# Performance work log

Measured on AMD Instinct MI355X. Metric: run time of the kernel, lower is better.

The kernel has to match this reference:

```python
import jax, jax.numpy as jnp
import numpy as np

B, S, D, H = 4, 4096, 2048, 256
GAMMA = 1.05


def setup_inputs() -> dict:
    key = jax.random.key(0)
    k1, k2, k3, k4 = jax.random.split(key, 4)
    X = jax.random.normal(k1, (B, S, D), dtype=jnp.float32)
    # nn.Linear(d_model, head_size) weights, stored as (in, out) for x @ W
    scale = 1.0 / np.sqrt(D)
    Wq = jax.random.normal(k2, (D, H), dtype=jnp.float32) * scale
    Wk = jax.random.normal(k3, (D, H), dtype=jnp.float32) * scale
    Wv = jax.random.normal(k4, (D, H), dtype=jnp.float32) * scale
    # decay = log(gamma * ones(head_size))
    decay = jnp.full((H,), np.log(GAMMA), dtype=jnp.float32)
    return {"X": X, "Wq": Wq, "Wk": Wk, "Wv": Wv, "decay": decay}


def reference(X, Wq, Wk, Wv, decay):
    # parallel (training) form of RetNet retention
    b, s, _ = X.shape
    h = Wq.shape[1]
    Q = jnp.einsum('bsd,dh->bsh', X, Wq)
    K = jnp.einsum('bsd,dh->bsh', X, Wk)
    V = jnp.einsum('bsd,dh->bsh', X, Wv)
    idx = jnp.arange(s)
    dist = jnp.abs(idx[:, None] - idx[None, :]).astype(X.dtype)  # [S,S]
    # scalar decay (all head_size entries identical at init; see notes)
    decay_matrix = jnp.exp(-decay[0] * dist)
    causal = jnp.tril(jnp.ones((s, s), dtype=X.dtype))
    decay_matrix = decay_matrix * causal
    scores = jnp.einsum('bsh,bth->bst', Q, K) * decay_matrix  # [B,S,S]
    scores = scores / jnp.asarray(h ** 0.5, dtype=X.dtype)
    out = jnp.einsum('bst,bth->bsh', scores, V)  # [B,S,H]
    return out
```

## Files before the change

kernel.cpp:

```cpp
#include <hip/hip_runtime.h>


typedef unsigned short u16;
typedef __attribute__((ext_vector_type(8))) short bf16x8;
typedef __attribute__((ext_vector_type(4))) float f32x4;

#define S_LEN 4096
#define DMODEL 2048
#define HSZ 256
#define NQKV 768
#define WINDOW 128
#define NT 32

__device__ __forceinline__ u16 f2bf(float f) {
  union { float f; unsigned u; } v; v.f = f;
  unsigned r = v.u + 0x7FFFu + ((v.u >> 16) & 1u);
  return (u16)(r >> 16);
}

__device__ __forceinline__ unsigned cvt2(float lo, float hi) {
  unsigned r;
  asm("v_cvt_pk_bf16_f32 %0, %1, %2" : "=v"(r) : "v"(lo), "v"(hi));
  return r;
}

__device__ __forceinline__ void glds16(const void* g, void* l) {
  __builtin_amdgcn_global_load_lds(
      (const __attribute__((address_space(1))) unsigned int*)g,
      (__attribute__((address_space(3))) unsigned int*)l, 16, 0, 0);
}

#define BAR() __builtin_amdgcn_s_barrier()
#define LGKM0() do { asm volatile("s_waitcnt lgkmcnt(0)" ::: "memory"); \
                     __builtin_amdgcn_sched_barrier(0); } while (0)
#define VM6() do { asm volatile("s_waitcnt vmcnt(6)" ::: "memory"); \
                   __builtin_amdgcn_sched_barrier(0); } while (0)
#define VM2() do { asm volatile("s_waitcnt vmcnt(2)" ::: "memory"); \
                   __builtin_amdgcn_sched_barrier(0); } while (0)
#define VM0() do { asm volatile("s_waitcnt vmcnt(0)" ::: "memory"); \
                   __builtin_amdgcn_sched_barrier(0); } while (0)

__global__ __launch_bounds__(256) void k_transposeW(const float* __restrict__ Wq,
                                                    const float* __restrict__ Wk,
                                                    const float* __restrict__ Wv,
                                                    u16* __restrict__ Wt) {
  __shared__ float s[32][33];
  int bid = blockIdx.x;
  int nt = bid % 24, kt = bid / 24;
  int n0 = nt * 32, k0 = kt * 32;
  const float* W = (n0 < 256) ? Wq : (n0 < 512 ? Wk : Wv);
  int nc = n0 & 255;
  int tx = threadIdx.x & 31, ty = threadIdx.x >> 5;
#pragma unroll
  for (int j = 0; j < 4; j++)
    s[ty + j * 8][tx] = W[(k0 + ty + j * 8) * HSZ + nc + tx];
  __syncthreads();
#pragma unroll
  for (int j = 0; j < 4; j++) {
    int nl = ty + j * 8;
    Wt[(n0 + nl) * DMODEL + k0 + tx] = f2bf(s[tx][nl]);
  }
}

__device__ __forceinline__ bf16x8 ldf(const char* hbase, int r, int ks) {
  return *(const bf16x8*)(hbase + r * 128 + ((ks ^ (r & 7)) << 4));
}
__device__ __forceinline__ void stageB(const u16* Bsrc, char* bufbase, int t,
                                       int cb, int w, int l) {
  int r0 = l >> 3, sl = (l & 7) ^ r0;
  glds16(Bsrc + (size_t)(cb * 64 + w * 8 + r0) * DMODEL + t * 64 + sl * 8,
         bufbase + cb * 8192 + w * 1024);
}
__device__ __forceinline__ void stageA(const float* __restrict__ X, size_t m0,
                                       char* slot, int t, int p, int j,
                                       int w, int l) {
#pragma unroll
  for (int i = 0; i < 2; i++) {
    int call = j * 16 + w * 2 + i;
    int sr = call * 4 + (l >> 4);
    int gs = (l & 15) ^ (sr & 15);
    int grow = ((sr >> 6) << 7) + p * 64 + (sr & 63);
    glds16(X + (m0 + (size_t)grow) * DMODEL + t * 64 + gs * 4,
           slot + call * 1024);
  }
}
__device__ __forceinline__ void readA(const char* slot, int wm, int c, int g,
                                      bf16x8 (&af)[4][2]) {
#pragma unroll
  for (int m = 0; m < 4; m++) {
    int sr = wm * 64 + m * 16 + c;
    const char* rowp = slot + sr * 256;
    int sw = sr & 15;
#pragma unroll
    for (int kc = 0; kc < 2; kc++) {
      int gb = kc * 8 + g * 2;
      float4 fa = *(const float4*)(rowp + ((gb) ^ sw) * 16);
      float4 fb = *(const float4*)(rowp + ((gb + 1) ^ sw) * 16);
      union { bf16x8 v; unsigned u[4]; } o;
      o.u[0] = cvt2(fa.x, fa.y);
      o.u[1] = cvt2(fa.z, fa.w);
      o.u[2] = cvt2(fb.x, fb.y);
      o.u[3] = cvt2(fb.z, fb.w);
      af[m][kc] = o.v;
    }
  }
}
__device__ __forceinline__ void read_b01(const char* Bc, int wn, int c, int g,
                                         bf16x8 (&dst)[2][2]) {
#pragma unroll
  for (int n = 0; n < 2; n++) {
    int r = wn * 48 + n * 16 + c;
    dst[n][0] = ldf(Bc, r, g);
    dst[n][1] = ldf(Bc, r, 4 + g);
  }
}
__device__ __forceinline__ void read_b2(const char* Bc, int wn, int c, int g,
                                        bf16x8 (&dst)[2]) {
  int r = wn * 48 + 32 + c;
  dst[0] = ldf(Bc, r, g);
  dst[1] = ldf(Bc, r, 4 + g);
}
__device__ __forceinline__ void mfma16(const bf16x8 (&A)[4][2], const bf16x8 (&Bf)[2][2],
                                       f32x4 (&acc)[8][3], int mo) {
  __builtin_amdgcn_s_setprio(1);
#pragma unroll
  for (int m = 0; m < 4; m++)
#pragma unroll
    for (int n = 0; n < 2; n++)
#pragma unroll
      for (int k = 0; k < 2; k++)
        acc[m + mo][n] = __builtin_amdgcn_mfma_f32_16x16x32_bf16(
            A[m][k], Bf[n][k], acc[m + mo][n], 0, 0, 0);
  __builtin_amdgcn_s_setprio(0);
}
__device__ __forceinline__ void mfma8(const bf16x8 (&A)[4][2], const bf16x8 (&Bf)[2],
                                      f32x4 (&acc)[8][3], int mo) {
  __builtin_amdgcn_s_setprio(1);
#pragma unroll
  for (int m = 0; m < 4; m++)
#pragma unroll
    for (int k = 0; k < 2; k++)
      acc[m + mo][2] = __builtin_amdgcn_mfma_f32_16x16x32_bf16(
          A[m][k], Bf[k], acc[m + mo][2], 0, 0, 0);
  __builtin_amdgcn_s_setprio(0);
}

__global__ __launch_bounds__(512, 1) void k_gemm(const float* __restrict__ X,
                                                 const u16* __restrict__ Wt,
                                                 u16* __restrict__ QKV) {
  __shared__ __attribute__((aligned(16))) char lds[147456];
  int tid = threadIdx.x;
  int w = tid >> 6, l = tid & 63, g = l >> 4, c = l & 15;
  int wm = w >> 2, wn = w & 3;
  int swz = (blockIdx.x & 7) * 32 + (blockIdx.x >> 3);
  int bm = swz & 63, bn = swz >> 6;
  size_t m0 = (size_t)bm * 256, n0 = (size_t)bn * 192;
  const u16* Bsrc = Wt + n0 * DMODEL;
  char* sA0 = lds;
  char* sA1 = lds + 32768;
  char* sA2 = lds + 65536;
#define BBUF(b) (lds + 98304 + (b) * 24576)

  f32x4 acc[8][3];
#pragma unroll
  for (int i = 0; i < 8; i++)
#pragma unroll
    for (int j = 0; j < 3; j++) acc[i][j] = (f32x4){0.f, 0.f, 0.f, 0.f};

  stageA(X, m0, sA0, 0, 0, 0, w, l);
  stageA(X, m0, sA0, 0, 0, 1, w, l);
  stageA(X, m0, sA1, 0, 1, 0, w, l);
  stageA(X, m0, sA1, 0, 1, 1, w, l);
  stageB(Bsrc, BBUF(0), 0, 0, w, l);
  stageB(Bsrc, BBUF(0), 0, 1, w, l);
  stageB(Bsrc, BBUF(0), 0, 2, w, l);
  VM0();
  BAR();

  bf16x8 af[4][2], bf01[2][2], bf2[2];
  for (int u = 0; u < NT; u++) {
    bool pre = (u + 1 < NT);
    char* Bc = BBUF(u & 1);
    char* Bn = BBUF((u + 1) & 1);
    readA(sA0, wm, c, g, af);
    read_b01(Bc, wn, c, g, bf01);
    if (pre) { stageA(X, m0, sA2, u + 1, 0, 0, w, l);
               stageB(Bsrc, Bn, u + 1, 0, w, l); }
    LGKM0();
    mfma16(af, bf01, acc, 0);
    BAR();
    read_b2(Bc, wn, c, g, bf2);
    if (pre) { stageA(X, m0, sA2, u + 1, 0, 1, w, l);
               stageB(Bsrc, Bn, u + 1, 1, w, l); }
    LGKM0();
    mfma8(af, bf2, acc, 0);
    if (pre) { VM6(); } else { VM0(); }
    BAR();
    readA(sA1, wm, c, g, af);
    if (pre) { stageA(X, m0, sA0, u + 1, 1, 0, w, l);
               stageB(Bsrc, Bn, u + 1, 2, w, l); }
    LGKM0();
    mfma8(af, bf2, acc, 4);
    BAR();
    if (pre) stageA(X, m0, sA0, u + 1, 1, 1, w, l);
    mfma16(af, bf01, acc, 4);
    if (pre) { VM2(); } else { VM0(); }
    BAR();
    char* t0 = sA0; sA0 = sA2; sA2 = sA1; sA1 = t0;
  }

#pragma unroll
  for (int fm = 0; fm < 8; fm++)
#pragma unroll
    for (int fn = 0; fn < 3; fn++)
#pragma unroll
      for (int r = 0; r < 4; r++) {
        size_t row = m0 + wm * 128 + fm * 16 + g * 4 + r;
        size_t col = n0 + wn * 48 + fn * 16 + c;
        QKV[row * NQKV + col] = f2bf(acc[fm][fn][r]);
      }
}

__global__ __launch_bounds__(256) void k_transposeV(const u16* __restrict__ QKV,
                                                    u16* __restrict__ Vt) {
  __shared__ __attribute__((aligned(16))) u16 s[64 * 72];
  int bid = blockIdx.x;
  int ht = bid & 3, st = (bid >> 2) & 63, b = bid >> 8;
  int s0 = st * 64, h0 = ht * 64;
  int tid = threadIdx.x;
#pragma unroll
  for (int i = 0; i < 2; i++) {
    int gr = i * 256 + tid;
    int rs = gr >> 3, cg = gr & 7;
    uint4 v = *(const uint4*)(QKV + (size_t)(b * S_LEN + s0 + rs) * NQKV + 512 + h0 + cg * 8);
    *(uint4*)(s + rs * 72 + cg * 8) = v;
  }
  __syncthreads();
#pragma unroll
  for (int i = 0; i < 2; i++) {
    int gr = i * 256 + tid;
    int hr = gr >> 3, cg = gr & 7;
    u16 u[8];
#pragma unroll
    for (int j = 0; j < 8; j++) u[j] = s[(cg * 8 + j) * 72 + hr];
    uint4 o;
    o.x = u[0] | ((unsigned)u[1] << 16);
    o.y = u[2] | ((unsigned)u[3] << 16);
    o.z = u[4] | ((unsigned)u[5] << 16);
    o.w = u[6] | ((unsigned)u[7] << 16);
    *(uint4*)(Vt + (size_t)b * (HSZ * S_LEN) + (size_t)(h0 + hr) * S_LEN + s0 + cg * 8) = o;
  }
}

__device__ __forceinline__ void attn_stage(const u16* __restrict__ QKV,
                                           const u16* __restrict__ Vt,
                                           int b, int t0, char* sK, char* sV, int tg) {
#pragma unroll
  for (int i = 0; i < 8; i++) {
    int gr = i * 256 + tg;
    {
      int row = gr >> 5, cg = gr & 31;
      uint4 v = *(const uint4*)(QKV + (size_t)(b * S_LEN + t0 + row) * NQKV + 256 + cg * 8);
      *(uint4*)(sK + ((row * 512 + cg * 16) ^ ((row & 7) << 4))) = v;
    }
    {
      int h = gr >> 3, cg = gr & 7;
      uint4 v = *(const uint4*)(Vt + (size_t)b * (HSZ * S_LEN) + (size_t)h * S_LEN + t0 + cg * 8);
      *(uint4*)(sV + ((h * 128 + cg * 16) ^ ((h & 7) << 4))) = v;
    }
  }
}

__device__ __forceinline__ void attn_compute(const char* sK, const char* sV,
                                             u16* sPw, const bf16x8 (&qf)[8],
                                             f32x4 (&acc)[16], int s0, int t0,
                                             int wq, int g, int c, float cl,
                                             const float (&bk)[4]) {
  f32x4 z = {0.f, 0.f, 0.f, 0.f};
  f32x4 sc[4];
  sc[0] = z; sc[1] = z; sc[2] = z; sc[3] = z;
#pragma unroll
  for (int f = 0; f < 4; f++) {
    int row = f * 16 + c;
    int rb = row * 512, sw = (row & 7) << 4;
#pragma unroll
    for (int kc = 0; kc < 8; kc++) {
      bf16x8 kf = *(const bf16x8*)(sK + ((rb + kc * 64 + g * 16) ^ sw));
      sc[f] = __builtin_amdgcn_mfma_f32_16x16x32_bf16(qf[kc], kf, sc[f], 0, 0, 0);
    }
  }
  int qb = s0 + wq * 16 + g * 4;
  int dt = qb - t0;
  float ar[4];
#pragma unroll
  for (int r = 0; r < 4; r++) ar[r] = __expf(cl * (float)(dt + r)) * 0.0625f;
#pragma unroll
  for (int f = 0; f < 4; f++) {
#pragma unroll
    for (int r = 0; r < 4; r++) {
      float p = sc[f][r] * ar[r] * bk[f];
      p = (dt + r - f * 16 - c >= 0) ? p : 0.f;
      sPw[(g * 4 + r) * 72 + f * 16 + c] = f2bf(p);
    }
  }
  bf16x8 pa[2];
#pragma unroll
  for (int kc = 0; kc < 2; kc++)
    pa[kc] = *(const bf16x8*)(sPw + c * 72 + kc * 32 + g * 8);
#pragma unroll
  for (int of = 0; of < 16; of++) {
#pragma unroll
    for (int kc = 0; kc < 2; kc++) {
      int hr = of * 16 + c;
      bf16x8 vf = *(const bf16x8*)(sV + ((hr * 128 + kc * 64 + g * 16) ^ ((hr & 7) << 4)));
      acc[of] = __builtin_amdgcn_mfma_f32_16x16x32_bf16(pa[kc], vf, acc[of], 0, 0, 0);
    }
  }
}

__global__ __launch_bounds__(512, 2) void k_attn(const u16* __restrict__ QKV,
                                                 const u16* __restrict__ Vt,
                                                 const float* __restrict__ decay,
                                                 float* __restrict__ out) {
  __shared__ __attribute__((aligned(16))) char smem[140288];
  int logical = (blockIdx.x & 7) * 32 + (blockIdx.x >> 3);
  int b = logical >> 6, qt = logical & 63, s0 = qt * 64;
  int tid = threadIdx.x, wid = tid >> 6, l = tid & 63, g = l >> 4, c = l & 15;
  int gid = wid >> 2, wq = wid & 3, tg = tid & 255;
  float cl = -decay[0];

  bf16x8 qf[8];
  const u16* qrow = QKV + (size_t)(b * S_LEN + s0 + wq * 16 + c) * NQKV;
#pragma unroll
  for (int kc = 0; kc < 8; kc++) qf[kc] = *(const bf16x8*)(qrow + kc * 32 + g * 8);

  float bk[4];
#pragma unroll
  for (int f = 0; f < 4; f++) bk[f] = __expf(-cl * (float)(f * 16 + c));

  f32x4 acc[16];
#pragma unroll
  for (int i = 0; i < 16; i++) acc[i] = (f32x4){0.f, 0.f, 0.f, 0.f};

  int tlo = s0 - WINDOW; if (tlo < 0) tlo = 0; tlo >>= 6;
  int ntiles = qt - tlo + 1;

  if (gid == 1) attn_stage(QKV, Vt, b, tlo * 64, smem, smem + 32768, tg);
  __syncthreads();
  for (int k = 0; k < ntiles; k++) {
    int bsel = k & 1;
    char* kb = smem + bsel * 65536;
    if ((k & 1) == gid) {
      attn_compute(kb, kb + 32768, (u16*)(smem + 131072) + wq * 16 * 72,
                   qf, acc, s0, (tlo + k) * 64, wq, g, c, cl, bk);
    } else if (tlo + k + 1 <= qt) {
      char* kb2 = smem + (bsel ^ 1) * 65536;
      attn_stage(QKV, Vt, b, (tlo + k + 1) * 64, kb2, kb2 + 32768, tg);
    }
    __syncthreads();
  }

  float* sO = (float*)smem;
  if (gid == 1) {
#pragma unroll
    for (int of = 0; of < 16; of++)
#pragma unroll
      for (int r = 0; r < 4; r++)
        sO[(wq * 16 + g * 4 + r) * 256 + of * 16 + c] = acc[of][r];
  }
  __syncthreads();
  if (gid == 0) {
    float* orow = out + (size_t)(b * S_LEN + s0 + wq * 16 + g * 4) * HSZ;
#pragma unroll
    for (int of = 0; of < 16; of++)
#pragma unroll
      for (int r = 0; r < 4; r++)
        orow[(size_t)r * HSZ + of * 16 + c] =
            acc[of][r] + sO[(wq * 16 + g * 4 + r) * 256 + of * 16 + c];
  }
}

extern "C" void kernel_launch(void* const* d_in, const int* in_sizes, int n_in,
                              void* d_out, int out_size, void* d_ws, size_t ws_size,
                              hipStream_t stream) {
  const float* X     = (const float*)d_in[0];
  const float* Wq    = (const float*)d_in[1];
  const float* Wk    = (const float*)d_in[2];
  const float* Wv    = (const float*)d_in[3];
  const float* decay = (const float*)d_in[4];
  float* out = (float*)d_out;

  char* ws = (char*)d_ws;
  u16* Wt  = (u16*)ws;
  u16* QKV = (u16*)(ws + 3145728);
  u16* Vt  = (u16*)(ws + 3145728 + 25165824);

  k_transposeW<<<1536, 256, 0, stream>>>(Wq, Wk, Wv, Wt);
  k_gemm      <<<256,  512, 0, stream>>>(X, Wt, QKV);
  k_transposeV<<<1024, 256, 0, stream>>>(QKV, Vt);
  k_attn      <<<256,  512, 0, stream>>>(QKV, Vt, decay, out);
}
```

Measured before the change: 114.6 us.

## Reshape GEMM warp tiling to 4x2 so each warp converts fewer A fragments

The QKV projection GEMM moves from a 2x4 warp grid (each warp 128x48) to a 4x2 grid (each warp 64x96). Each warp now reads and converts one fp32 A fragment set per k-step instead of two, at the cost of reading more B fragments. The A tile is staged as two contiguous 128-row halves. The per-iteration schedule is rebuilt with fewer barriers and new vmcnt waits (4 and 1), which changes the overlap of global-to-LDS loads with MFMA work.

```diff
diff --git a/kernel.cpp b/kernel.cpp
--- a/kernel.cpp
+++ b/kernel.cpp
@@ -33,9 +33,9 @@
 #define BAR() __builtin_amdgcn_s_barrier()
 #define LGKM0() do { asm volatile("s_waitcnt lgkmcnt(0)" ::: "memory"); \
                      __builtin_amdgcn_sched_barrier(0); } while (0)
-#define VM6() do { asm volatile("s_waitcnt vmcnt(6)" ::: "memory"); \
+#define VM4() do { asm volatile("s_waitcnt vmcnt(4)" ::: "memory"); \
                    __builtin_amdgcn_sched_barrier(0); } while (0)
-#define VM2() do { asm volatile("s_waitcnt vmcnt(2)" ::: "memory"); \
+#define VM1() do { asm volatile("s_waitcnt vmcnt(1)" ::: "memory"); \
                    __builtin_amdgcn_sched_barrier(0); } while (0)
 #define VM0() do { asm volatile("s_waitcnt vmcnt(0)" ::: "memory"); \
                    __builtin_amdgcn_sched_barrier(0); } while (0)
@@ -71,24 +71,25 @@
   glds16(Bsrc + (size_t)(cb * 64 + w * 8 + r0) * DMODEL + t * 64 + sl * 8,
          bufbase + cb * 8192 + w * 1024);
 }
-__device__ __forceinline__ void stageA(const float* __restrict__ X, size_t m0,
-                                       char* slot, int t, int p, int j,
-                                       int w, int l) {
-#pragma unroll
-  for (int i = 0; i < 2; i++) {
-    int call = j * 16 + w * 2 + i;
-    int sr = call * 4 + (l >> 4);
-    int gs = (l & 15) ^ (sr & 15);
-    int grow = ((sr >> 6) << 7) + p * 64 + (sr & 63);
-    glds16(X + (m0 + (size_t)grow) * DMODEL + t * 64 + gs * 4,
-           slot + call * 1024);
-  }
-}
-__device__ __forceinline__ void readA(const char* slot, int wm, int c, int g,
+__device__ __forceinline__ void stageAhalf(const float* __restrict__ X, size_t m0,
+                                           int rowoff, char* slot, int t,
+                                           int w, int l) {
+#pragma unroll
+  for (int jp = 0; jp < 2; jp++)
+#pragma unroll
+    for (int i = 0; i < 2; i++) {
+      int call = jp * 16 + w * 2 + i;
+      int sr = call * 4 + (l >> 4);
+      int gs = (l & 15) ^ (sr & 15);
+      glds16(X + (m0 + (size_t)(rowoff + sr)) * DMODEL + t * 64 + gs * 4,
+             slot + call * 1024);
+    }
+}
+__device__ __forceinline__ void readA(const char* slot, int wmh, int c, int g,
                                       bf16x8 (&af)[4][2]) {
 #pragma unroll
   for (int m = 0; m < 4; m++) {
-    int sr = wm * 64 + m * 16 + c;
+    int sr = wmh * 64 + m * 16 + c;
     const char* rowp = slot + sr * 256;
     int sw = sr & 15;
 #pragma unroll
@@ -105,23 +106,23 @@
     }
   }
 }
-__device__ __forceinline__ void read_b01(const char* Bc, int wn, int c, int g,
-                                         bf16x8 (&dst)[2][2]) {
+__device__ __forceinline__ void read_bpair(const char* Bc, int wn, int fnb,
+                                           int c, int g, bf16x8 (&dst)[2][2]) {
 #pragma unroll
   for (int n = 0; n < 2; n++) {
-    int r = wn * 48 + n * 16 + c;
+    int r = wn * 96 + (fnb + n) * 16 + c;
     dst[n][0] = ldf(Bc, r, g);
     dst[n][1] = ldf(Bc, r, 4 + g);
   }
 }
-__device__ __forceinline__ void read_b2(const char* Bc, int wn, int c, int g,
-                                        bf16x8 (&dst)[2]) {
-  int r = wn * 48 + 32 + c;
+__device__ __forceinline__ void read_bone(const char* Bc, int wn, int fn,
+                                          int c, int g, bf16x8 (&dst)[2]) {
+  int r = wn * 96 + fn * 16 + c;
   dst[0] = ldf(Bc, r, g);
   dst[1] = ldf(Bc, r, 4 + g);
 }
 __device__ __forceinline__ void mfma16(const bf16x8 (&A)[4][2], const bf16x8 (&Bf)[2][2],
-                                       f32x4 (&acc)[8][3], int mo) {
+                                       f32x4 (&acc)[4][6], int no) {
   __builtin_amdgcn_s_setprio(1);
 #pragma unroll
   for (int m = 0; m < 4; m++)
@@ -129,19 +130,19 @@
     for (int n = 0; n < 2; n++)
 #pragma unroll
       for (int k = 0; k < 2; k++)
-        acc[m + mo][n] = __builtin_amdgcn_mfma_f32_16x16x32_bf16(
-            A[m][k], Bf[n][k], acc[m + mo][n], 0, 0, 0);
+        acc[m][no + n] = __builtin_amdgcn_mfma_f32_16x16x32_bf16(
+            A[m][k], Bf[n][k], acc[m][no + n], 0, 0, 0);
   __builtin_amdgcn_s_setprio(0);
 }
 __device__ __forceinline__ void mfma8(const bf16x8 (&A)[4][2], const bf16x8 (&Bf)[2],
-                                      f32x4 (&acc)[8][3], int mo) {
+                                      f32x4 (&acc)[4][6], int fn) {
   __builtin_amdgcn_s_setprio(1);
 #pragma unroll
   for (int m = 0; m < 4; m++)
 #pragma unroll
     for (int k = 0; k < 2; k++)
-      acc[m + mo][2] = __builtin_amdgcn_mfma_f32_16x16x32_bf16(
-          A[m][k], Bf[k], acc[m + mo][2], 0, 0, 0);
+      acc[m][fn] = __builtin_amdgcn_mfma_f32_16x16x32_bf16(
+          A[m][k], Bf[k], acc[m][fn], 0, 0, 0);
   __builtin_amdgcn_s_setprio(0);
 }
 
@@ -151,7 +152,8 @@
   __shared__ __attribute__((aligned(16))) char lds[147456];
   int tid = threadIdx.x;
   int w = tid >> 6, l = tid & 63, g = l >> 4, c = l & 15;
-  int wm = w >> 2, wn = w & 3;
+  int wm = w >> 1, wn = w & 1;
+  int wmh = wm & 1;
   int swz = (blockIdx.x & 7) * 32 + (blockIdx.x >> 3);
   int bm = swz & 63, bn = swz >> 6;
   size_t m0 = (size_t)bm * 256, n0 = (size_t)bn * 192;
@@ -161,62 +163,59 @@
   char* sA2 = lds + 65536;
 #define BBUF(b) (lds + 98304 + (b) * 24576)
 
-  f32x4 acc[8][3];
-#pragma unroll
-  for (int i = 0; i < 8; i++)
-#pragma unroll
-    for (int j = 0; j < 3; j++) acc[i][j] = (f32x4){0.f, 0.f, 0.f, 0.f};
-
-  stageA(X, m0, sA0, 0, 0, 0, w, l);
-  stageA(X, m0, sA0, 0, 0, 1, w, l);
-  stageA(X, m0, sA1, 0, 1, 0, w, l);
-  stageA(X, m0, sA1, 0, 1, 1, w, l);
+  f32x4 acc[4][6];
+#pragma unroll
+  for (int i = 0; i < 4; i++)
+#pragma unroll
+    for (int j = 0; j < 6; j++) acc[i][j] = (f32x4){0.f, 0.f, 0.f, 0.f};
+
+  stageAhalf(X, m0, 0,   sA0, 0, w, l);
+  stageAhalf(X, m0, 128, sA1, 0, w, l);
   stageB(Bsrc, BBUF(0), 0, 0, w, l);
   stageB(Bsrc, BBUF(0), 0, 1, w, l);
   stageB(Bsrc, BBUF(0), 0, 2, w, l);
   VM0();
   BAR();
 
-  bf16x8 af[4][2], bf01[2][2], bf2[2];
+  bf16x8 af[4][2], bf[2][2], bs[2];
   for (int u = 0; u < NT; u++) {
     bool pre = (u + 1 < NT);
     char* Bc = BBUF(u & 1);
     char* Bn = BBUF((u + 1) & 1);
-    readA(sA0, wm, c, g, af);
-    read_b01(Bc, wn, c, g, bf01);
-    if (pre) { stageA(X, m0, sA2, u + 1, 0, 0, w, l);
-               stageB(Bsrc, Bn, u + 1, 0, w, l); }
+    const char* Aslot = (wm < 2) ? sA0 : sA1;
+    readA(Aslot, wmh, c, g, af);
+    read_bpair(Bc, wn, 0, c, g, bf);
+    if (pre) stageAhalf(X, m0, 0, sA2, u + 1, w, l);
     LGKM0();
-    mfma16(af, bf01, acc, 0);
+    mfma16(af, bf, acc, 0);
+    if (pre) { VM4(); } else { VM0(); }
     BAR();
-    read_b2(Bc, wn, c, g, bf2);
-    if (pre) { stageA(X, m0, sA2, u + 1, 0, 1, w, l);
+    read_bpair(Bc, wn, 2, c, g, bf);
+    if (pre) stageAhalf(X, m0, 128, sA0, u + 1, w, l);
+    LGKM0();
+    mfma16(af, bf, acc, 2);
+    read_bone(Bc, wn, 4, c, g, bs);
+    if (pre) { stageB(Bsrc, Bn, u + 1, 0, w, l);
                stageB(Bsrc, Bn, u + 1, 1, w, l); }
     LGKM0();
-    mfma8(af, bf2, acc, 0);
-    if (pre) { VM6(); } else { VM0(); }
-    BAR();
-    readA(sA1, wm, c, g, af);
-    if (pre) { stageA(X, m0, sA0, u + 1, 1, 0, w, l);
-               stageB(Bsrc, Bn, u + 1, 2, w, l); }
+    mfma8(af, bs, acc, 4);
+    read_bone(Bc, wn, 5, c, g, bs);
+    if (pre) stageB(Bsrc, Bn, u + 1, 2, w, l);
     LGKM0();
-    mfma8(af, bf2, acc, 4);
-    BAR();
-    if (pre) stageA(X, m0, sA0, u + 1, 1, 1, w, l);
-    mfma16(af, bf01, acc, 4);
-    if (pre) { VM2(); } else { VM0(); }
+    mfma8(af, bs, acc, 5);
+    if (pre) VM1();
     BAR();
     char* t0 = sA0; sA0 = sA2; sA2 = sA1; sA1 = t0;
   }
 
 #pragma unroll
-  for (int fm = 0; fm < 8; fm++)
-#pragma unroll
-    for (int fn = 0; fn < 3; fn++)
+  for (int fm = 0; fm < 4; fm++)
+#pragma unroll
+    for (int fn = 0; fn < 6; fn++)
 #pragma unroll
       for (int r = 0; r < 4; r++) {
-        size_t row = m0 + wm * 128 + fm * 16 + g * 4 + r;
-        size_t col = n0 + wn * 48 + fn * 16 + c;
+        size_t row = m0 + wm * 64 + fm * 16 + g * 4 + r;
+        size_t col = n0 + wn * 96 + fn * 16 + c;
         QKV[row * NQKV + col] = f2bf(acc[fm][fn][r]);
       }
 }
```

After: 125.3 us. 1.09x slower.

## Convert X tiles to bf16 once in LDS instead of per-warp in registers

Applied to the files above, without the earlier changes.

Adds a cooperative pass in which each thread converts a slice of the staged fp32 X tile into a swizzled bf16 LDS buffer. The MFMA warps then read bf16 fragments directly, so the four N-warps no longer each redo the fp32 loads and conversions. The three-slot fp32 ring becomes two fp32 staging buffers plus two bf16 buffers, and the barrier and vmcnt schedule is reworked around them. The cost is an extra LDS write/read pass and a full vmcnt(0) wait at the end of every iteration, which shortens how far loads can be prefetched ahead.

```diff
diff --git a/kernel.cpp b/kernel.cpp
--- a/kernel.cpp
+++ b/kernel.cpp
@@ -33,9 +33,7 @@
 #define BAR() __builtin_amdgcn_s_barrier()
 #define LGKM0() do { asm volatile("s_waitcnt lgkmcnt(0)" ::: "memory"); \
                      __builtin_amdgcn_sched_barrier(0); } while (0)
-#define VM6() do { asm volatile("s_waitcnt vmcnt(6)" ::: "memory"); \
-                   __builtin_amdgcn_sched_barrier(0); } while (0)
-#define VM2() do { asm volatile("s_waitcnt vmcnt(2)" ::: "memory"); \
+#define VM7() do { asm volatile("s_waitcnt vmcnt(7)" ::: "memory"); \
                    __builtin_amdgcn_sched_barrier(0); } while (0)
 #define VM0() do { asm volatile("s_waitcnt vmcnt(0)" ::: "memory"); \
                    __builtin_amdgcn_sched_barrier(0); } while (0)
@@ -71,38 +69,40 @@
   glds16(Bsrc + (size_t)(cb * 64 + w * 8 + r0) * DMODEL + t * 64 + sl * 8,
          bufbase + cb * 8192 + w * 1024);
 }
-__device__ __forceinline__ void stageA(const float* __restrict__ X, size_t m0,
-                                       char* slot, int t, int p, int j,
-                                       int w, int l) {
-#pragma unroll
-  for (int i = 0; i < 2; i++) {
-    int call = j * 16 + w * 2 + i;
+__device__ __forceinline__ void stageF32(const float* __restrict__ X, size_t m0,
+                                         int qoff, char* slot, int t,
+                                         int w, int l) {
+#pragma unroll
+  for (int j = 0; j < 4; j++) {
+    int call = w * 4 + j;
     int sr = call * 4 + (l >> 4);
     int gs = (l & 15) ^ (sr & 15);
-    int grow = ((sr >> 6) << 7) + p * 64 + (sr & 63);
+    int grow = ((sr >> 6) << 7) + qoff + (sr & 63);
     glds16(X + (m0 + (size_t)grow) * DMODEL + t * 64 + gs * 4,
            slot + call * 1024);
   }
 }
-__device__ __forceinline__ void readA(const char* slot, int wm, int c, int g,
-                                      bf16x8 (&af)[4][2]) {
+__device__ __forceinline__ void convQ(const char* f32G, char* b16G, int tid) {
+  int sr = tid >> 2;
+  int p0 = (tid & 3) * 4;
+#pragma unroll
+  for (int i = 0; i < 4; i++) {
+    int p = p0 + i;
+    f32x4 v = *(const f32x4*)(f32G + sr * 256 + p * 16);
+    int s = p ^ (sr & 15);
+    uint2 o;
+    o.x = cvt2(v.x, v.y);
+    o.y = cvt2(v.z, v.w);
+    *(uint2*)(b16G + sr * 128 + ((((s >> 1) ^ (sr & 7)) << 4) + (s & 1) * 8)) = o;
+  }
+}
+__device__ __forceinline__ void readAbf(const char* b16G, int wm, int c, int g,
+                                        bf16x8 (&af)[4][2]) {
 #pragma unroll
   for (int m = 0; m < 4; m++) {
-    int sr = wm * 64 + m * 16 + c;
-    const char* rowp = slot + sr * 256;
-    int sw = sr & 15;
-#pragma unroll
-    for (int kc = 0; kc < 2; kc++) {
-      int gb = kc * 8 + g * 2;
-      float4 fa = *(const float4*)(rowp + ((gb) ^ sw) * 16);
-      float4 fb = *(const float4*)(rowp + ((gb + 1) ^ sw) * 16);
-      union { bf16x8 v; unsigned u[4]; } o;
-      o.u[0] = cvt2(fa.x, fa.y);
-      o.u[1] = cvt2(fa.z, fa.w);
-      o.u[2] = cvt2(fb.x, fb.y);
-      o.u[3] = cvt2(fb.z, fb.w);
-      af[m][kc] = o.v;
-    }
+    int r = wm * 64 + m * 16 + c;
+    af[m][0] = ldf(b16G, r, g);
+    af[m][1] = ldf(b16G, r, 4 + g);
   }
 }
 __device__ __forceinline__ void read_b01(const char* Bc, int wn, int c, int g,
@@ -156,9 +156,10 @@
   int bm = swz & 63, bn = swz >> 6;
   size_t m0 = (size_t)bm * 256, n0 = (size_t)bn * 192;
   const u16* Bsrc = Wt + n0 * DMODEL;
-  char* sA0 = lds;
-  char* sA1 = lds + 32768;
-  char* sA2 = lds + 65536;
+  char* f32A = lds;
+  char* f32B = lds + 32768;
+  char* b16A = lds + 65536;
+  char* b16B = lds + 81920;
 #define BBUF(b) (lds + 98304 + (b) * 24576)
 
   f32x4 acc[8][3];
@@ -167,46 +168,44 @@
 #pragma unroll
     for (int j = 0; j < 3; j++) acc[i][j] = (f32x4){0.f, 0.f, 0.f, 0.f};
 
-  stageA(X, m0, sA0, 0, 0, 0, w, l);
-  stageA(X, m0, sA0, 0, 0, 1, w, l);
-  stageA(X, m0, sA1, 0, 1, 0, w, l);
-  stageA(X, m0, sA1, 0, 1, 1, w, l);
+  stageF32(X, m0, 0,  f32A, 0, w, l);
+  stageF32(X, m0, 64, f32B, 0, w, l);
   stageB(Bsrc, BBUF(0), 0, 0, w, l);
   stageB(Bsrc, BBUF(0), 0, 1, w, l);
   stageB(Bsrc, BBUF(0), 0, 2, w, l);
   VM0();
   BAR();
-
-  bf16x8 af[4][2], bf01[2][2], bf2[2];
+  convQ(f32A, b16A, tid);
+  LGKM0();
+  BAR();
+
+  bf16x8 af[4][2], bf01[2][2], bs[2];
   for (int u = 0; u < NT; u++) {
     bool pre = (u + 1 < NT);
     char* Bc = BBUF(u & 1);
     char* Bn = BBUF((u + 1) & 1);
-    readA(sA0, wm, c, g, af);
+    readAbf(b16A, wm, c, g, af);
     read_b01(Bc, wn, c, g, bf01);
-    if (pre) { stageA(X, m0, sA2, u + 1, 0, 0, w, l);
-               stageB(Bsrc, Bn, u + 1, 0, w, l); }
+    if (pre) stageF32(X, m0, 0, f32A, u + 1, w, l);
     LGKM0();
     mfma16(af, bf01, acc, 0);
-    BAR();
-    read_b2(Bc, wn, c, g, bf2);
-    if (pre) { stageA(X, m0, sA2, u + 1, 0, 1, w, l);
-               stageB(Bsrc, Bn, u + 1, 1, w, l); }
-    LGKM0();
-    mfma8(af, bf2, acc, 0);
-    if (pre) { VM6(); } else { VM0(); }
-    BAR();
-    readA(sA1, wm, c, g, af);
-    if (pre) { stageA(X, m0, sA0, u + 1, 1, 0, w, l);
+    read_b2(Bc, wn, c, g, bs);
+    convQ(f32B, b16B, tid);
+    if (pre) { stageB(Bsrc, Bn, u + 1, 0, w, l);
+               stageB(Bsrc, Bn, u + 1, 1, w, l);
                stageB(Bsrc, Bn, u + 1, 2, w, l); }
     LGKM0();
-    mfma8(af, bf2, acc, 4);
+    mfma8(af, bs, acc, 0);
     BAR();
-    if (pre) stageA(X, m0, sA0, u + 1, 1, 1, w, l);
+    readAbf(b16B, wm, c, g, af);
+    if (pre) stageF32(X, m0, 64, f32B, u + 1, w, l);
+    LGKM0();
+    mfma8(af, bs, acc, 4);
+    if (pre) { VM7(); convQ(f32A, b16A, tid); }
     mfma16(af, bf01, acc, 4);
-    if (pre) { VM2(); } else { VM0(); }
+    LGKM0();
+    VM0();
     BAR();
-    char* t0 = sA0; sA0 = sA2; sA2 = sA1; sA1 = t0;
   }
 
 #pragma unroll
```

After: 115.6 us. About the same (+1.0%).
